# Performance work log

Measured on AMD Instinct MI355X. Metric: run time of the kernel, lower is better.

Reference implementation:

```python
import jax, jax.numpy as jnp
import numpy as np

B, T, F, H = 4096, 8, 64, 64          # batch(=edges), time windows, feat_dim, attention hidden
N, De = 2048, 128                      # graph nodes, node/edge feature dim
NF, NC = 64, 2                         # conv filters, num classes
HID1, HID2 = 256, 24                   # LazyLinear dims
FLAT = NF * T * 2 * F                  # flattened conv output


def setup_inputs() -> dict:
    key = jax.random.key(0)
    ks = jax.random.split(key, 25)
    rn = lambda k, shape, s=0.05: jax.random.normal(k, shape, jnp.float32) * s
    return {
        "X_nume": jax.random.normal(ks[0], (B, T, F), jnp.float32),
        "src": jax.random.randint(ks[1], (B,), 0, N, jnp.int32),
        "dst": jax.random.randint(ks[2], (B,), 0, N, jnp.int32),
        "node_feat": jax.random.normal(ks[3], (N, De), jnp.float32),
        "edge_feat": jax.random.normal(ks[4], (B, De), jnp.float32),
        # attention params (original uses uniform(0,1); scaled uniform here)
        "attn_W": jax.random.uniform(ks[5], (F, H), jnp.float32) * 0.1,
        "attn_U": jax.random.uniform(ks[6], (F, H), jnp.float32) * 0.1,
        "attn_V": jax.random.uniform(ks[7], (H, 1), jnp.float32) * 0.1,
        # conv
        "conv_w": rn(ks[8], (NF, 1, 2, 2)), "conv_b": rn(ks[9], (NF,)),
        # GraphConv 1/2 (weights stored [in, out])
        "gc1_W": rn(ks[10], (De, 128)), "gc1_b": rn(ks[11], (128,)),
        "gc2_W": rn(ks[12], (128, 8)), "gc2_b": rn(ks[13], (8,)),
        # edge linears
        "lin1_W": rn(ks[14], (De, 128)), "lin1_b": rn(ks[15], (128,)),
        "lin2_W": rn(ks[16], (128, 8)), "lin2_b": rn(ks[17], (8,)),
        # MLP head
        "fc1_W": rn(ks[18], (FLAT, HID1), 0.01), "fc1_b": rn(ks[19], (HID1,)),
        "fc2_W": rn(ks[20], (HID1, HID2)), "fc2_b": rn(ks[21], (HID2,)),
        "fc3_W": rn(ks[22], (HID2 + 24, NC)), "fc3_b": rn(ks[23], (NC,)),
    }


def _graph_conv(h, W, b, src, dst, n):
    # DGL GraphConv, norm='both': out = D_in^{-1/2} A D_out^{-1/2} h W + b
    ones = jnp.ones(src.shape[0], h.dtype)
    deg_out = jnp.clip(jax.ops.segment_sum(ones, src, num_segments=n), 1.0)
    deg_in = jnp.clip(jax.ops.segment_sum(ones, dst, num_segments=n), 1.0)
    hs = h * jax.lax.rsqrt(deg_out)[:, None]
    agg = jax.ops.segment_sum(hs[src], dst, num_segments=n)  # [N, in]
    agg = agg * jax.lax.rsqrt(deg_in)[:, None]
    return agg @ W + b


def _forward(X_nume, src, dst, node_feat, edge_feat,
             attn_W, attn_U, attn_V, conv_w, conv_b,
             gc1_W, gc1_b, gc2_W, gc2_b, lin1_W, lin1_b, lin2_W, lin2_b,
             fc1_W, fc1_b, fc2_W, fc2_b, fc3_W, fc3_b):
    # ---- temporal attention (vectorized O(T^2)) ----
    a = jnp.einsum('btf,fh->bth', X_nume, attn_W)   # x_i W
    u = jnp.einsum('btf,fh->bth', X_nume, attn_U)   # x_j U
    # e[b,i,j] = tanh(a_i + u_j) @ V  -> [B,T,T]
    e = jnp.einsum('bijh,h->bij', jnp.tanh(a[:, :, None, :] + u[:, None, :, :]), attn_V[:, 0])
    alpha = jax.nn.softmax(e, axis=2)
    # c_i = sum_{j != i} alpha_ij x_j  (softmax over all j, self term excluded from sum)
    ctx = jnp.einsum('bij,bjf->bif', alpha, X_nume)
    diag = jnp.diagonal(alpha, axis1=1, axis2=2)    # [B,T]
    ctx = ctx - diag[:, :, None] * X_nume
    att_out = jnp.concatenate([X_nume, ctx], axis=-1)  # [B,T,2F]

    # ---- CNN ----
    conv_in = att_out[:, None, :, :]  # [B,1,T,2F]
    conv_out = jax.lax.conv_general_dilated(
        conv_in, conv_w, window_strides=(1, 1), padding='SAME',
        dimension_numbers=('NCHW', 'OIHW', 'NCHW')) + conv_b[None, :, None, None]
    conv_out = jax.nn.relu(conv_out)  # [B,NF,T,2F]

    # ---- dual GraphConv message passing ----
    h1 = jax.nn.relu(_graph_conv(node_feat, gc1_W, gc1_b, src, dst, N))
    e1 = jax.nn.relu(edge_feat @ lin1_W + lin1_b)
    h2 = _graph_conv(h1, gc2_W, gc2_b, src, dst, N)   # no relu (matches source)
    e2 = jax.nn.relu(e1 @ lin2_W + lin2_b)
    edge_x = h2[src] + h2[dst] + e2                    # [E,8]
    node_feats = jnp.stack([h2[src], h2[dst], edge_x], axis=1).reshape(B, -1)  # [B,24]

    # ---- MLP head ----
    out = conv_out.reshape(B, -1)
    out = jax.nn.relu(out @ fc1_W + fc1_b)
    out = jax.nn.relu(out @ fc2_W + fc2_b)
    out = jnp.concatenate([out, node_feats], axis=1)
    return out @ fc3_W + fc3_b  # [B, NC]


def reference(X_nume, src, dst, node_feat, edge_feat,
              attn_W, attn_U, attn_V, conv_w, conv_b,
              gc1_W, gc1_b, gc2_W, gc2_b, lin1_W, lin1_b, lin2_W, lin2_b,
              fc1_W, fc1_b, fc2_W, fc2_b, fc3_W, fc3_b):
    return _forward(X_nume, src, dst, node_feat, edge_feat,
                    attn_W, attn_U, attn_V, conv_w, conv_b,
                    gc1_W, gc1_b, gc2_W, gc2_b, lin1_W, lin1_b, lin2_W, lin2_b,
                    fc1_W, fc1_b, fc2_W, fc2_b, fc3_W, fc3_b)
```

## Files before the change

kernel.cpp:

```cpp
#include <hip/hip_runtime.h>
#include <stdint.h>
#include <stddef.h>

typedef float    f32x4  __attribute__((ext_vector_type(4)));
typedef short    bf16x8 __attribute__((ext_vector_type(8)));
typedef uint16_t u16x8  __attribute__((ext_vector_type(8)));
typedef uint32_t u32x4  __attribute__((ext_vector_type(4)));

#define ATT_ROW 136

__device__ __forceinline__ uint16_t f2bf(float x) {
  union { float f; uint32_t u; } c; c.f = x;
  return (uint16_t)((c.u + 0x7FFFu + ((c.u >> 16) & 1u)) >> 16);
}
__device__ __forceinline__ float bf2f(uint16_t h) {
  union { uint32_t u; float f; } c; c.u = ((uint32_t)h) << 16;
  return c.f;
}
__device__ __forceinline__ int S64s(int a) { return a ^ (((a >> 6) & 7) << 4); }

__device__ __forceinline__ float fast_tanh(float t) {
  float r = __expf(-2.f * t);
  return 1.f - 2.f * r / (1.f + r);
}

__global__ __launch_bounds__(256) void k_prep(const float* __restrict__ W1,
                                              uint16_t* __restrict__ W1s) {
  __shared__ float st[32 * 256];
  const int c = blockIdx.x, tid = threadIdx.x;
  const float* src = W1 + (size_t)c * 32 * 256;
#pragma unroll
  for (int it = 0; it < 8; ++it) {
    int u = it * 256 + tid;
    ((f32x4*)st)[u] = ((const f32x4*)src)[u];
  }
  __syncthreads();
  uint16_t* dstc = W1s + (size_t)c * 8192;
#pragma unroll
  for (int q = 0; q < 4; ++q) {
    int p  = q * 256 + tid;
    int Np = p >> 2, Gp = p & 3;
    int n  = Np ^ ((Np >> 2) & 1);
    int g  = Gp ^ (n & 3);
    uint32_t w[4];
#pragma unroll
    for (int e2 = 0; e2 < 4; ++e2) {
      uint16_t lo = f2bf(st[(g * 8 + 2 * e2) * 256 + n]);
      uint16_t hi = f2bf(st[(g * 8 + 2 * e2 + 1) * 256 + n]);
      w[e2] = (uint32_t)lo | ((uint32_t)hi << 16);
    }
    u32x4 v; v.x = w[0]; v.y = w[1]; v.z = w[2]; v.w = w[3];
    *(u32x4*)(dstc + (size_t)p * 8) = v;
  }
}

__global__ __launch_bounds__(512) void k_att(const float* __restrict__ X,
    const float* __restrict__ aW, const float* __restrict__ aU,
    const float* __restrict__ aV, uint16_t* __restrict__ att) {
  __shared__ float sa[8][8][66];
  __shared__ float su[8][8][66];
  __shared__ float sal[8][64];
  __shared__ float sv[64];
  const int tid = threadIdx.x, lane = tid & 63, w = tid >> 6;
  if (tid < 64) sv[tid] = aV[tid];
  __syncthreads();
  for (int rep = 0; rep < 2; ++rep) {
    int b  = blockIdx.x * 16 + w * 2 + rep;
    int bu = __builtin_amdgcn_readfirstlane(b);
    const float* xb = X + (size_t)bu * 512;
    float xi[8];
#pragma unroll
    for (int i = 0; i < 8; ++i) xi[i] = xb[i * 64 + lane];
    float a[8], u[8];
#pragma unroll
    for (int i = 0; i < 8; ++i) { a[i] = 0.f; u[i] = 0.f; }
#pragma unroll
    for (int f = 0; f < 64; ++f) {
      float wf = aW[f * 64 + lane];
      float uf = aU[f * 64 + lane];
#pragma unroll
      for (int i = 0; i < 8; ++i) {
        float xs = xb[i * 64 + f];
        a[i] = fmaf(xs, wf, a[i]);
        u[i] = fmaf(xs, uf, u[i]);
      }
    }
#pragma unroll
    for (int i = 0; i < 8; ++i) { sa[w][i][lane] = a[i]; su[w][i][lane] = u[i]; }
    __syncthreads();
    int i2 = lane >> 3, j2 = lane & 7;
    float ev = 0.f;
#pragma unroll
    for (int h = 0; h < 64; ++h)
      ev = fmaf(fast_tanh(sa[w][i2][h] + su[w][j2][h]), sv[h], ev);
    float m = ev;
    m = fmaxf(m, __shfl_xor(m, 1));
    m = fmaxf(m, __shfl_xor(m, 2));
    m = fmaxf(m, __shfl_xor(m, 4));
    float p = __expf(ev - m);
    float s = p;
    s += __shfl_xor(s, 1); s += __shfl_xor(s, 2); s += __shfl_xor(s, 4);
    sal[w][lane] = p / s;
    __syncthreads();
#pragma unroll
    for (int i = 0; i < 8; ++i) {
      float c = 0.f;
#pragma unroll
      for (int j = 0; j < 8; ++j) c = fmaf(sal[w][i * 8 + j], xi[j], c);
      c = fmaf(-sal[w][i * 8 + i], xi[i], c);
      size_t ro = ((size_t)b * 9 + i) * ATT_ROW;
      att[ro + lane]      = f2bf(xi[i]);
      att[ro + 64 + lane] = f2bf(c);
      if (lane < 8) att[ro + 128 + lane] = 0;
    }
    {
      size_t ro = ((size_t)b * 9 + 8) * ATT_ROW;
      att[ro + lane] = 0; att[ro + 64 + lane] = 0;
      if (lane < 8) att[ro + 128 + lane] = 0;
    }
    __syncthreads();
  }
}

__global__ void k_deg(const int* __restrict__ src, const int* __restrict__ dst,
                      float* degO, float* degI) {
  int t = blockIdx.x * 256 + threadIdx.x;
  if (t < 4096) {
    atomicAdd(degO + src[t], 1.f);
    atomicAdd(degI + dst[t], 1.f);
  }
}
__global__ __launch_bounds__(256) void k_gca(const float* __restrict__ h,
    const int* __restrict__ src, const int* __restrict__ dst,
    const float* __restrict__ degO, float* __restrict__ agg) {
  int t = blockIdx.x * 256 + threadIdx.x;
  int e = t >> 7, d = t & 127;
  int s = src[e];
  float sc = rsqrtf(fmaxf(degO[s], 1.f));
  atomicAdd(agg + (size_t)dst[e] * 128 + d, h[(size_t)s * 128 + d] * sc);
}
__global__ __launch_bounds__(128) void k_gc1b(const float* __restrict__ agg,
    const float* __restrict__ degI, const float* __restrict__ Wt,
    const float* __restrict__ bs, float* __restrict__ h1) {
  __shared__ float vs[128];
  int n = blockIdx.x, t = threadIdx.x;
  float sc = rsqrtf(fmaxf(degI[n], 1.f));
  vs[t] = agg[(size_t)n * 128 + t] * sc;
  __syncthreads();
  float acc = bs[t];
#pragma unroll 8
  for (int d = 0; d < 128; ++d) acc = fmaf(vs[d], Wt[d * 128 + t], acc);
  h1[(size_t)n * 128 + t] = fmaxf(acc, 0.f);
}
__global__ __launch_bounds__(128) void k_gc2b(const float* __restrict__ agg,
    const float* __restrict__ degI, const float* __restrict__ Wt,
    const float* __restrict__ bs, float* __restrict__ h2) {
  __shared__ float vs[128];
  int n = blockIdx.x, t = threadIdx.x;
  float sc = rsqrtf(fmaxf(degI[n], 1.f));
  vs[t] = agg[(size_t)n * 128 + t] * sc;
  __syncthreads();
  if (t < 8) {
    float acc = bs[t];
#pragma unroll 8
    for (int d = 0; d < 128; ++d) acc = fmaf(vs[d], Wt[d * 8 + t], acc);
    h2[(size_t)n * 8 + t] = acc;
  }
}
__global__ __launch_bounds__(128) void k_e12(const float* __restrict__ ef,
    const float* __restrict__ W1, const float* __restrict__ b1,
    const float* __restrict__ W2, const float* __restrict__ b2,
    float* __restrict__ e2) {
  __shared__ float efs[128];
  __shared__ float t1s[128];
  int t = threadIdx.x;
  for (int it = 0; it < 16; ++it) {
    int b = blockIdx.x * 16 + it;
    efs[t] = ef[(size_t)b * 128 + t];
    __syncthreads();
    float acc = b1[t];
#pragma unroll 8
    for (int d = 0; d < 128; ++d) acc = fmaf(efs[d], W1[d * 128 + t], acc);
    t1s[t] = fmaxf(acc, 0.f);
    __syncthreads();
    if (t < 8) {
      float a2 = b2[t];
#pragma unroll 8
      for (int h = 0; h < 128; ++h) a2 = fmaf(t1s[h], W2[h * 8 + t], a2);
      e2[(size_t)b * 8 + t] = fmaxf(a2, 0.f);
    }
    __syncthreads();
  }
}

__global__ __launch_bounds__(512) void k_gemm(const uint16_t* __restrict__ W1s,
    const uint16_t* __restrict__ att, const float* __restrict__ conv_w,
    const float* __restrict__ conv_b, float* __restrict__ out1) {
  __shared__ __align__(16) char smem[32768];

  const int tid = threadIdx.x;
  const int lane = tid & 63, ln15 = lane & 15, g = lane >> 4;
  const int wid = tid >> 6, wm = wid >> 2, wvn = wid & 3;
  const int bid = blockIdx.x;
  const int i_row = bid & 7, oh = (bid >> 3) & 1;
  const int btile = bid >> 4;
  const int b0 = btile * 128;
  const int am = tid >> 2, ag = tid & 3;

  const uint16_t* rb = att + ((size_t)(b0 + am) * 9 + i_row) * ATT_ROW + ag * 16;
  const char* W1c = (const char*)W1s + ((size_t)(oh * 32) * 32 + i_row * 4) * 16384;
  int voff[4], aro[4];
#pragma unroll
  for (int nt = 0; nt < 4; ++nt)
    voff[nt] = S64s((wvn * 64 + nt * 16 + ln15) * 64 + g * 16);
#pragma unroll
  for (int mt = 0; mt < 4; ++mt)
    aro[mt] = S64s((wm * 64 + mt * 16 + ln15) * 64 + g * 16);
  const int aw0 = (ag >> 1) * 8192 + S64s(am * 64 + (ag & 1) * 32);

  f32x4 acc[4][4];
#pragma unroll
  for (int mt = 0; mt < 4; ++mt)
#pragma unroll
    for (int nt = 0; nt < 4; ++nt) { f32x4 z = {0.f, 0.f, 0.f, 0.f}; acc[mt][nt] = z; }

  struct Win { u16x8 a0, a1, b0, b1; uint16_t ae, be; };
  auto loadWin = [&](int h) {
    const uint16_t* r0 = rb + h * 64;
    const uint16_t* r1 = r0 + ATT_ROW;
    Win w;
    w.a0 = *(const u16x8*)r0; w.a1 = *(const u16x8*)(r0 + 8); w.ae = r0[16];
    w.b0 = *(const u16x8*)r1; w.b1 = *(const u16x8*)(r1 + 8); w.be = r1[16];
    return w;
  };

  auto computeA = [&](const Win& w, int o, char* As) {
    float t0[17], t1[17];
#pragma unroll
    for (int e = 0; e < 8; ++e) {
      t0[e] = bf2f((uint16_t)w.a0[e]); t0[e + 8] = bf2f((uint16_t)w.a1[e]);
      t1[e] = bf2f((uint16_t)w.b0[e]); t1[e + 8] = bf2f((uint16_t)w.b1[e]);
    }
    t0[16] = bf2f(w.ae); t1[16] = bf2f(w.be);
    float c0  = conv_b[o];
    float k00 = conv_w[o * 4 + 0], k01 = conv_w[o * 4 + 1];
    float k10 = conv_w[o * 4 + 2], k11 = conv_w[o * 4 + 3];
    uint32_t pk[8];
#pragma unroll
    for (int e2 = 0; e2 < 16; e2 += 2) {
      float v0 = fmaf(k00, t0[e2],     fmaf(k01, t0[e2 + 1], fmaf(k10, t1[e2],     fmaf(k11, t1[e2 + 1], c0))));
      float v1 = fmaf(k00, t0[e2 + 1], fmaf(k01, t0[e2 + 2], fmaf(k10, t1[e2 + 1], fmaf(k11, t1[e2 + 2], c0))));
      v0 = fmaxf(v0, 0.f); v1 = fmaxf(v1, 0.f);
      uint32_t pr;
      asm("v_cvt_pk_bf16_f32 %0, %1, %2" : "=v"(pr) : "v"(v0), "v"(v1));
      pk[e2 >> 1] = pr;
    }
    u32x4 wv0; wv0.x = pk[0]; wv0.y = pk[1]; wv0.z = pk[2]; wv0.w = pk[3];
    u32x4 wv1; wv1.x = pk[4]; wv1.y = pk[5]; wv1.z = pk[6]; wv1.w = pk[7];
    *(u32x4*)(As + aw0)        = wv0;
    *(u32x4*)(As + (aw0 ^ 16)) = wv1;
  };

  auto mfmaStep = [&](const char* As, const bf16x8* bank) {
#pragma unroll
    for (int kk = 0; kk < 2; ++kk) {
      bf16x8 afr[4];
#pragma unroll
      for (int mt = 0; mt < 4; ++mt)
        afr[mt] = *(const bf16x8*)(As + kk * 8192 + aro[mt]);
#pragma unroll
      for (int mt = 0; mt < 4; ++mt)
#pragma unroll
        for (int nt = 0; nt < 4; ++nt)
          acc[mt][nt] = __builtin_amdgcn_mfma_f32_16x16x32_bf16(afr[mt], bank[kk * 4 + nt], acc[mt][nt], 0, 0, 0);
    }
  };

  bf16x8 bA[8], bB[8];
  Win winC, winN;

#pragma unroll
  for (int nt = 0; nt < 4; ++nt) {
    bA[nt]     = *(const bf16x8*)(W1c + voff[nt]);
    bA[4 + nt] = *(const bf16x8*)(W1c + 16384 + voff[nt]);
  }
  {
    Win w0 = loadWin(0);
    computeA(w0, oh * 32, smem);
  }
  winC = loadWin(1);
  winN = winC;
  asm volatile("s_waitcnt lgkmcnt(0)" ::: "memory");
  __builtin_amdgcn_sched_barrier(0);
  __builtin_amdgcn_s_barrier();
  __builtin_amdgcn_sched_barrier(0);

#define GEMM_STEP(CUR, NXT, CB1, H2, O1, ARD, AWR, DO_L)                         \
  {                                                                              \
    _Pragma("unroll") for (int nt = 0; nt < 4; ++nt) {                           \
      NXT[nt]     = *(const bf16x8*)((CB1) + voff[nt]);                          \
      NXT[4 + nt] = *(const bf16x8*)((CB1) + 16384 + voff[nt]);                  \
    }                                                                            \
    if (DO_L) winN = loadWin(H2);                                                \
    computeA(winC, (O1), (AWR));                                                 \
    winC = winN;                                                                 \
    mfmaStep((ARD), CUR);                                                        \
    asm volatile("s_waitcnt lgkmcnt(0)" ::: "memory");                           \
    __builtin_amdgcn_sched_barrier(0);                                           \
    __builtin_amdgcn_s_barrier();                                                \
    __builtin_amdgcn_sched_barrier(0);                                           \
  }

  const char* cb = W1c;
  int oc = oh * 32;
#pragma unroll 1
  for (int it = 0; it < 31; ++it) {
    GEMM_STEP(bA, bB, cb + 32768, 0, oc, smem, smem + 16384, 1)
    GEMM_STEP(bB, bA, cb + 524288, 1, oc + 1, smem + 16384, smem, 1)
    cb += 524288;
    ++oc;
  }
  {
#pragma unroll
    for (int nt = 0; nt < 4; ++nt) {
      bB[nt]     = *(const bf16x8*)(cb + 32768 + voff[nt]);
      bB[4 + nt] = *(const bf16x8*)(cb + 32768 + 16384 + voff[nt]);
    }
    computeA(winC, oh * 32 + 31, smem + 16384);
    mfmaStep(smem, bA);
    asm volatile("s_waitcnt lgkmcnt(0)" ::: "memory");
    __builtin_amdgcn_sched_barrier(0);
    __builtin_amdgcn_s_barrier();
    __builtin_amdgcn_sched_barrier(0);
  }
  mfmaStep(smem + 16384, bB);
#undef GEMM_STEP

  const int rbase = b0 + wm * 64 + (lane >> 4) * 4;
  const int cbase = wvn * 64 + ln15;
#pragma unroll
  for (int mt = 0; mt < 4; ++mt)
#pragma unroll
    for (int nt = 0; nt < 4; ++nt)
#pragma unroll
      for (int r = 0; r < 4; ++r)
        atomicAdd(out1 + (size_t)(rbase + mt * 16 + r) * 256 + cbase + nt * 16,
                  acc[mt][nt][r]);
}

__global__ __launch_bounds__(512) void k_fin(const float* __restrict__ out1,
    const float* __restrict__ fc1_b, const float* __restrict__ fc2_W,
    const float* __restrict__ fc2_b, const float* __restrict__ fc3_W,
    const float* __restrict__ fc3_b, const int* __restrict__ src,
    const int* __restrict__ dst, const float* __restrict__ h2,
    const float* __restrict__ e2, float* __restrict__ outp) {
  int lane = threadIdx.x & 63, w = threadIdx.x >> 6;
  int b  = blockIdx.x * 8 + w;
  int bu = __builtin_amdgcn_readfirstlane(b);
  f32x4 o4 = ((const f32x4*)(out1 + (size_t)bu * 256))[lane];
  f32x4 bi = ((const f32x4*)fc1_b)[lane];
  float v[4];
#pragma unroll
  for (int r = 0; r < 4; ++r) v[r] = fmaxf(o4[r] + bi[r], 0.f);
  float a24[24];
#pragma unroll
  for (int q = 0; q < 24; ++q) a24[q] = 0.f;
#pragma unroll
  for (int r = 0; r < 4; ++r) {
    const float* wr = fc2_W + (size_t)(lane * 4 + r) * 24;
#pragma unroll
    for (int q = 0; q < 24; ++q) a24[q] = fmaf(v[r], wr[q], a24[q]);
  }
#pragma unroll
  for (int q = 0; q < 24; ++q) {
    float t = a24[q];
    t += __shfl_xor(t, 1);  t += __shfl_xor(t, 2);  t += __shfl_xor(t, 4);
    t += __shfl_xor(t, 8);  t += __shfl_xor(t, 16); t += __shfl_xor(t, 32);
    a24[q] = fmaxf(t + fc2_b[q], 0.f);
  }
  int s = src[bu], d2 = dst[bu];
  float nf[24];
#pragma unroll
  for (int q = 0; q < 8; ++q) {
    float hs = h2[(size_t)s * 8 + q];
    float hd = h2[(size_t)d2 * 8 + q];
    nf[q] = hs; nf[8 + q] = hd; nf[16 + q] = hs + hd + e2[(size_t)bu * 8 + q];
  }
  if (lane == 0) {
#pragma unroll
    for (int c = 0; c < 2; ++c) {
      float r = fc3_b[c];
#pragma unroll
      for (int q = 0; q < 24; ++q) r = fmaf(a24[q], fc3_W[q * 2 + c], r);
#pragma unroll
      for (int q = 0; q < 24; ++q) r = fmaf(nf[q], fc3_W[(24 + q) * 2 + c], r);
      outp[(size_t)bu * 2 + c] = r;
    }
  }
}

extern "C" void kernel_launch(void* const* d_in, const int* in_sizes, int n_in,
                              void* d_out, int out_size, void* d_ws, size_t ws_size,
                              hipStream_t stream) {
  const float* X         = (const float*)d_in[0];
  const int*   src       = (const int*)d_in[1];
  const int*   dst       = (const int*)d_in[2];
  const float* node_feat = (const float*)d_in[3];
  const float* edge_feat = (const float*)d_in[4];
  const float* attn_W    = (const float*)d_in[5];
  const float* attn_U    = (const float*)d_in[6];
  const float* attn_V    = (const float*)d_in[7];
  const float* conv_w    = (const float*)d_in[8];
  const float* conv_b    = (const float*)d_in[9];
  const float* gc1_W     = (const float*)d_in[10];
  const float* gc1_b     = (const float*)d_in[11];
  const float* gc2_W     = (const float*)d_in[12];
  const float* gc2_b     = (const float*)d_in[13];
  const float* lin1_W    = (const float*)d_in[14];
  const float* lin1_b    = (const float*)d_in[15];
  const float* lin2_W    = (const float*)d_in[16];
  const float* lin2_b    = (const float*)d_in[17];
  const float* fc1_W     = (const float*)d_in[18];
  const float* fc1_b     = (const float*)d_in[19];
  const float* fc2_W     = (const float*)d_in[20];
  const float* fc2_b     = (const float*)d_in[21];
  const float* fc3_W     = (const float*)d_in[22];
  const float* fc3_b     = (const float*)d_in[23];

  char* ws = (char*)d_ws;
  float*    out1 = (float*)(ws + 0);
  float*    agg1 = (float*)(ws + 4194304);
  float*    agg2 = (float*)(ws + 5242880);
  float*    degO = (float*)(ws + 6291456);
  float*    degI = (float*)(ws + 6299648);
  uint16_t* W1s  = (uint16_t*)(ws + 6307840);
  uint16_t* att  = (uint16_t*)(ws + 39862272);
  float*    h1   = (float*)(ws + 49889280);
  float*    h2   = (float*)(ws + 50937856);
  float*    e2   = (float*)(ws + 51003392);

  hipMemsetAsync(d_ws, 0, 6307840, stream);

  k_prep<<<dim3(2048), dim3(256), 0, stream>>>(fc1_W, W1s);
  k_att <<<dim3(256),  dim3(512), 0, stream>>>(X, attn_W, attn_U, attn_V, att);
  k_deg <<<dim3(16),   dim3(256), 0, stream>>>(src, dst, degO, degI);
  k_gca <<<dim3(2048), dim3(256), 0, stream>>>(node_feat, src, dst, degO, agg1);
  k_gc1b<<<dim3(2048), dim3(128), 0, stream>>>(agg1, degI, gc1_W, gc1_b, h1);
  k_gca <<<dim3(2048), dim3(256), 0, stream>>>(h1, src, dst, degO, agg2);
  k_gc2b<<<dim3(2048), dim3(128), 0, stream>>>(agg2, degI, gc2_W, gc2_b, h2);
  k_e12 <<<dim3(256),  dim3(128), 0, stream>>>(edge_feat, lin1_W, lin1_b, lin2_W, lin2_b, e2);
  k_gemm<<<dim3(512),  dim3(512), 0, stream>>>(W1s, att, conv_w, conv_b, out1);
  k_fin <<<dim3(512),  dim3(512), 0, stream>>>(out1, fc1_b, fc2_W, fc2_b, fc3_W, fc3_b,
                                               src, dst, h2, e2, (float*)d_out);
}
```

Baseline: 520.4 us.

## Hoist loop-invariant attention windows and interleave conv compute with MFMA scheduling

The attention windows used to build the conv-activation tile are loop-invariant, so they are loaded once instead of reloaded every step. Conv parameters are prefetched one iteration ahead. LDS fragment reads are issued before the conv VALU work, and sched_group_barrier hints interleave MFMAs with VALU and LDS operations. The aim is to hide the VALU conv computation under matrix-core work and cut redundant global traffic, at the cost of higher register pressure.

Result: faster. 492.8 us (-5.3%).

```diff
diff --git a/kernel.cpp b/kernel.cpp
--- a/kernel.cpp
+++ b/kernel.cpp
@@ -6,6 +6,7 @@
 typedef short    bf16x8 __attribute__((ext_vector_type(8)));
 typedef uint16_t u16x8  __attribute__((ext_vector_type(8)));
 typedef uint32_t u32x4  __attribute__((ext_vector_type(4)));
+typedef const bf16x8 __attribute__((address_space(1))) *gcbf16x8;
 
 #define ATT_ROW 136
 
@@ -193,6 +194,9 @@
   }
 }
 
+struct CC { float c0, k00, k01, k10, k11; };
+struct Win { u16x8 a0, a1, b0, b1; uint16_t ae, be; };
+
 __global__ __launch_bounds__(512) void k_gemm(const uint16_t* __restrict__ W1s,
     const uint16_t* __restrict__ att, const float* __restrict__ conv_w,
     const float* __restrict__ conv_b, float* __restrict__ out1) {
@@ -224,7 +228,6 @@
 #pragma unroll
     for (int nt = 0; nt < 4; ++nt) { f32x4 z = {0.f, 0.f, 0.f, 0.f}; acc[mt][nt] = z; }
 
-  struct Win { u16x8 a0, a1, b0, b1; uint16_t ae, be; };
   auto loadWin = [&](int h) {
     const uint16_t* r0 = rb + h * 64;
     const uint16_t* r1 = r0 + ATT_ROW;
@@ -233,108 +236,111 @@
     w.b0 = *(const u16x8*)r1; w.b1 = *(const u16x8*)(r1 + 8); w.be = r1[16];
     return w;
   };
-
-  auto computeA = [&](const Win& w, int o, char* As) {
-    float t0[17], t1[17];
-#pragma unroll
-    for (int e = 0; e < 8; ++e) {
-      t0[e] = bf2f((uint16_t)w.a0[e]); t0[e + 8] = bf2f((uint16_t)w.a1[e]);
-      t1[e] = bf2f((uint16_t)w.b0[e]); t1[e + 8] = bf2f((uint16_t)w.b1[e]);
-    }
-    t0[16] = bf2f(w.ae); t1[16] = bf2f(w.be);
-    float c0  = conv_b[o];
-    float k00 = conv_w[o * 4 + 0], k01 = conv_w[o * 4 + 1];
-    float k10 = conv_w[o * 4 + 2], k11 = conv_w[o * 4 + 3];
-    uint32_t pk[8];
-#pragma unroll
-    for (int e2 = 0; e2 < 16; e2 += 2) {
-      float v0 = fmaf(k00, t0[e2],     fmaf(k01, t0[e2 + 1], fmaf(k10, t1[e2],     fmaf(k11, t1[e2 + 1], c0))));
-      float v1 = fmaf(k00, t0[e2 + 1], fmaf(k01, t0[e2 + 2], fmaf(k10, t1[e2 + 1], fmaf(k11, t1[e2 + 2], c0))));
-      v0 = fmaxf(v0, 0.f); v1 = fmaxf(v1, 0.f);
-      uint32_t pr;
-      asm("v_cvt_pk_bf16_f32 %0, %1, %2" : "=v"(pr) : "v"(v0), "v"(v1));
-      pk[e2 >> 1] = pr;
-    }
-    u32x4 wv0; wv0.x = pk[0]; wv0.y = pk[1]; wv0.z = pk[2]; wv0.w = pk[3];
-    u32x4 wv1; wv1.x = pk[4]; wv1.y = pk[5]; wv1.z = pk[6]; wv1.w = pk[7];
-    *(u32x4*)(As + aw0)        = wv0;
-    *(u32x4*)(As + (aw0 ^ 16)) = wv1;
+  auto loadCC = [&](int o) {
+    CC c; c.c0 = conv_b[o];
+    c.k00 = conv_w[o * 4 + 0]; c.k01 = conv_w[o * 4 + 1];
+    c.k10 = conv_w[o * 4 + 2]; c.k11 = conv_w[o * 4 + 3];
+    return c;
   };
 
-  auto mfmaStep = [&](const char* As, const bf16x8* bank) {
-#pragma unroll
-    for (int kk = 0; kk < 2; ++kk) {
-      bf16x8 afr[4];
-#pragma unroll
-      for (int mt = 0; mt < 4; ++mt)
-        afr[mt] = *(const bf16x8*)(As + kk * 8192 + aro[mt]);
-#pragma unroll
-      for (int mt = 0; mt < 4; ++mt)
-#pragma unroll
-        for (int nt = 0; nt < 4; ++nt)
-          acc[mt][nt] = __builtin_amdgcn_mfma_f32_16x16x32_bf16(afr[mt], bank[kk * 4 + nt], acc[mt][nt], 0, 0, 0);
-    }
-  };
+#define CA_BODY(WH, CCX, AWR)                                                      \
+  {                                                                                \
+    float t0[17], t1[17];                                                          \
+    _Pragma("unroll") for (int e = 0; e < 8; ++e) {                                \
+      t0[e] = bf2f((uint16_t)(WH).a0[e]); t0[e + 8] = bf2f((uint16_t)(WH).a1[e]);  \
+      t1[e] = bf2f((uint16_t)(WH).b0[e]); t1[e + 8] = bf2f((uint16_t)(WH).b1[e]);  \
+    }                                                                              \
+    t0[16] = bf2f((WH).ae); t1[16] = bf2f((WH).be);                                \
+    uint32_t pk[8];                                                                \
+    _Pragma("unroll") for (int e2 = 0; e2 < 16; e2 += 2) {                         \
+      float v0 = fmaf((CCX).k00, t0[e2], fmaf((CCX).k01, t0[e2 + 1],               \
+                 fmaf((CCX).k10, t1[e2], fmaf((CCX).k11, t1[e2 + 1], (CCX).c0)))); \
+      float v1 = fmaf((CCX).k00, t0[e2 + 1], fmaf((CCX).k01, t0[e2 + 2],           \
+                 fmaf((CCX).k10, t1[e2 + 1], fmaf((CCX).k11, t1[e2 + 2], (CCX).c0))));\
+      v0 = fmaxf(v0, 0.f); v1 = fmaxf(v1, 0.f);                                    \
+      uint32_t pr;                                                                 \
+      asm("v_cvt_pk_bf16_f32 %0, %1, %2" : "=v"(pr) : "v"(v0), "v"(v1));           \
+      pk[e2 >> 1] = pr;                                                            \
+    }                                                                              \
+    u32x4 wv0; wv0.x = pk[0]; wv0.y = pk[1]; wv0.z = pk[2]; wv0.w = pk[3];         \
+    u32x4 wv1; wv1.x = pk[4]; wv1.y = pk[5]; wv1.z = pk[6]; wv1.w = pk[7];         \
+    *(u32x4*)((AWR) + aw0)        = wv0;                                           \
+    *(u32x4*)((AWR) + (aw0 ^ 16)) = wv1;                                           \
+  }
+
+#define CSTEP(ARD, AWR, BANK, FILLB, FSRC, WH, CCX)                                \
+  {                                                                                \
+    _Pragma("unroll") for (int nt = 0; nt < 4; ++nt) {                             \
+      FILLB[nt]     = *(gcbf16x8)((FSRC) + voff[nt]);                              \
+      FILLB[4 + nt] = *(gcbf16x8)((FSRC) + 16384 + voff[nt]);                      \
+    }                                                                              \
+    bf16x8 afr[8];                                                                 \
+    _Pragma("unroll") for (int kk = 0; kk < 2; ++kk)                               \
+      _Pragma("unroll") for (int mt = 0; mt < 4; ++mt)                             \
+        afr[kk * 4 + mt] = *(const bf16x8*)((ARD) + kk * 8192 + aro[mt]);          \
+    CA_BODY(WH, CCX, AWR)                                                          \
+    _Pragma("unroll") for (int kk = 0; kk < 2; ++kk)                               \
+      _Pragma("unroll") for (int mt = 0; mt < 4; ++mt)                             \
+        _Pragma("unroll") for (int nt = 0; nt < 4; ++nt)                           \
+          acc[mt][nt] = __builtin_amdgcn_mfma_f32_16x16x32_bf16(                   \
+              afr[kk * 4 + mt], BANK[kk * 4 + nt], acc[mt][nt], 0, 0, 0);          \
+    __builtin_amdgcn_sched_group_barrier(0x20, 8, 0);         \
+    __builtin_amdgcn_sched_group_barrier(0x100, 8, 0);         \
+    _Pragma("unroll") for (int gq = 0; gq < 8; ++gq) {                             \
+      __builtin_amdgcn_sched_group_barrier(0x2, 14, 0);             \
+      __builtin_amdgcn_sched_group_barrier(0x8, 4, 0);              \
+    }                                                                              \
+    __builtin_amdgcn_sched_group_barrier(0x200, 2, 0);            \
+    asm volatile("s_waitcnt lgkmcnt(0)" ::: "memory");                             \
+    __builtin_amdgcn_sched_barrier(0);                                             \
+    __builtin_amdgcn_s_barrier();                                                  \
+    __builtin_amdgcn_sched_barrier(0);                                             \
+  }
 
   bf16x8 bA[8], bB[8];
-  Win winC, winN;
-
+
+  const Win wH0 = loadWin(0);
+  const Win wH1 = loadWin(1);
+  CC cc = loadCC(oh * 32);
 #pragma unroll
   for (int nt = 0; nt < 4; ++nt) {
-    bA[nt]     = *(const bf16x8*)(W1c + voff[nt]);
-    bA[4 + nt] = *(const bf16x8*)(W1c + 16384 + voff[nt]);
-  }
-  {
-    Win w0 = loadWin(0);
-    computeA(w0, oh * 32, smem);
-  }
-  winC = loadWin(1);
-  winN = winC;
+    bA[nt]     = *(gcbf16x8)(W1c + voff[nt]);
+    bA[4 + nt] = *(gcbf16x8)(W1c + 16384 + voff[nt]);
+  }
+  CA_BODY(wH0, cc, smem)
   asm volatile("s_waitcnt lgkmcnt(0)" ::: "memory");
   __builtin_amdgcn_sched_barrier(0);
   __builtin_amdgcn_s_barrier();
   __builtin_amdgcn_sched_barrier(0);
 
-#define GEMM_STEP(CUR, NXT, CB1, H2, O1, ARD, AWR, DO_L)                         \
-  {                                                                              \
-    _Pragma("unroll") for (int nt = 0; nt < 4; ++nt) {                           \
-      NXT[nt]     = *(const bf16x8*)((CB1) + voff[nt]);                          \
-      NXT[4 + nt] = *(const bf16x8*)((CB1) + 16384 + voff[nt]);                  \
-    }                                                                            \
-    if (DO_L) winN = loadWin(H2);                                                \
-    computeA(winC, (O1), (AWR));                                                 \
-    winC = winN;                                                                 \
-    mfmaStep((ARD), CUR);                                                        \
-    asm volatile("s_waitcnt lgkmcnt(0)" ::: "memory");                           \
-    __builtin_amdgcn_sched_barrier(0);                                           \
-    __builtin_amdgcn_s_barrier();                                                \
-    __builtin_amdgcn_sched_barrier(0);                                           \
-  }
-
   const char* cb = W1c;
-  int oc = oh * 32;
 #pragma unroll 1
   for (int it = 0; it < 31; ++it) {
-    GEMM_STEP(bA, bB, cb + 32768, 0, oc, smem, smem + 16384, 1)
-    GEMM_STEP(bB, bA, cb + 524288, 1, oc + 1, smem + 16384, smem, 1)
+    CC ccN = loadCC(oh * 32 + it + 1);
+    CSTEP(smem, smem + 16384, bA, bB, cb + 32768, wH1, cc)
+    CSTEP(smem + 16384, smem, bB, bA, cb + 524288, wH0, ccN)
+    cc = ccN;
     cb += 524288;
-    ++oc;
-  }
+  }
+  CSTEP(smem, smem + 16384, bA, bB, cb + 32768, wH1, cc)
   {
-#pragma unroll
-    for (int nt = 0; nt < 4; ++nt) {
-      bB[nt]     = *(const bf16x8*)(cb + 32768 + voff[nt]);
-      bB[4 + nt] = *(const bf16x8*)(cb + 32768 + 16384 + voff[nt]);
-    }
-    computeA(winC, oh * 32 + 31, smem + 16384);
-    mfmaStep(smem, bA);
-    asm volatile("s_waitcnt lgkmcnt(0)" ::: "memory");
-    __builtin_amdgcn_sched_barrier(0);
-    __builtin_amdgcn_s_barrier();
-    __builtin_amdgcn_sched_barrier(0);
-  }
-  mfmaStep(smem + 16384, bB);
-#undef GEMM_STEP
+    bf16x8 afr[8];
+#pragma unroll
+    for (int kk = 0; kk < 2; ++kk)
+#pragma unroll
+      for (int mt = 0; mt < 4; ++mt)
+        afr[kk * 4 + mt] = *(const bf16x8*)(smem + 16384 + kk * 8192 + aro[mt]);
+#pragma unroll
+    for (int kk = 0; kk < 2; ++kk)
+#pragma unroll
+      for (int mt = 0; mt < 4; ++mt)
+#pragma unroll
+        for (int nt = 0; nt < 4; ++nt)
+          acc[mt][nt] = __builtin_amdgcn_mfma_f32_16x16x32_bf16(
+              afr[kk * 4 + mt], bB[kk * 4 + nt], acc[mt][nt], 0, 0, 0);
+  }
+#undef CSTEP
+#undef CA_BODY
 
   const int rbase = b0 + wm * 64 + (lane >> 4) * 4;
   const int cbase = wvn * 64 + ln15;
```
